# Optimization experiments

Measured on AMD Instinct MI355X. Metric: run time of the kernel, lower is better.

Reference implementation:

```python
import jax, jax.numpy as jnp
import numpy as np

B, S, DIN, DOUT = 4, 2048, 2048, 8192


def setup_inputs() -> dict:
    key = jax.random.key(0)
    kx, kw = jax.random.split(key)
    x = jax.random.normal(kx, (B, S, DIN), dtype=jnp.float32)
    # match torch init: uniform(-bound, bound), bound = sqrt(3) * 0.5 * in_features**-0.5
    bound = (3.0 ** 0.5) * 0.5 * DIN ** (-0.5)
    weight = jax.random.uniform(kw, (DOUT, DIN), dtype=jnp.float32, minval=-bound, maxval=bound)
    return {"x": x, "weight": weight}


def _rms_norm(x):
    # F.rms_norm with no weight: eps defaults to finfo(dtype).eps
    eps = jnp.finfo(x.dtype).eps
    return x * jax.lax.rsqrt(jnp.mean(x * x, axis=-1, keepdims=True) + eps)


def _act_quant(xn):
    # per-token int8 symmetric quant/dequant
    scale = 127.0 / jnp.maximum(jnp.max(jnp.abs(xn), axis=-1, keepdims=True), 1e-5)
    return jnp.clip(jnp.round(xn * scale), -128.0, 127.0) / scale


def _weight_quant(w):
    # ternary weight quant/dequant with global abs-mean scale
    scale = 1.0 / jnp.maximum(jnp.mean(jnp.abs(w)), 1e-5)
    return jnp.clip(jnp.round(w * scale), -1.0, 1.0) / scale


def reference(x, weight):
    xn = _rms_norm(x)
    # STE: forward uses quantized values, gradient flows through xn / weight
    x_q = xn + jax.lax.stop_gradient(_act_quant(xn) - xn)
    w_q = weight + jax.lax.stop_gradient(_weight_quant(weight) - weight)
    # F.linear: x @ w.T  -> [B, S, DOUT]
    return jnp.einsum('bsd,od->bso', x_q, w_q)
```

## Files before the change

kernel.cpp:

```cpp
#include <hip/hip_runtime.h>

typedef unsigned int u32;
typedef int i32x4 __attribute__((ext_vector_type(4)));

#define DIN 2048
#define DOUT 8192
#define MROWS 8192
#define NELEM_W (8192 * 2048)
#define NT 16

#define WS_PART 0
#define WS_WFAC 16384
#define WS_ROWFAC 16640
#define WS_XQ 49408
#define WS_WQ (49408 + 16777216)

__global__ void k_wabs(const float* __restrict__ w, double* __restrict__ part) {
    const float4* w4 = (const float4*)w;
    const unsigned t = threadIdx.x, b = blockIdx.x;
    float s = 0.f;
    for (unsigned i = b * 256u + t; i < (NELEM_W / 4); i += 2048u * 256u) {
        float4 v = w4[i];
        s += fabsf(v.x) + fabsf(v.y) + fabsf(v.z) + fabsf(v.w);
    }
    double d = (double)s;
    #pragma unroll
    for (int o = 32; o; o >>= 1) d += __shfl_down(d, o);
    __shared__ double red[4];
    if ((t & 63u) == 0u) red[t >> 6] = d;
    __syncthreads();
    if (t == 0) part[b] = red[0] + red[1] + red[2] + red[3];
}

__global__ void k_wfin(const double* __restrict__ part, float* __restrict__ wfac) {
    const int t = threadIdx.x;
    double s = 0.0;
    #pragma unroll
    for (int j = 0; j < 8; ++j) s += part[t + j * 256];
    #pragma unroll
    for (int o = 32; o; o >>= 1) s += __shfl_down(s, o);
    __shared__ double red[4];
    if ((t & 63) == 0) red[t >> 6] = s;
    __syncthreads();
    if (t == 0) {
        double mean = (red[0] + red[1] + red[2] + red[3]) * (1.0 / (double)NELEM_W);
        *wfac = fmaxf((float)mean, 1e-5f);
    }
}

__global__ void k_prep(const float* __restrict__ w, const float* __restrict__ wfac,
                       u32* __restrict__ wq, const float* __restrict__ x,
                       u32* __restrict__ xq, float* __restrict__ rowfac) {
    const int t = threadIdx.x;
    if (blockIdx.x < 2048) {
        const float scale = 1.0f / *wfac;
        const float4* w4 = (const float4*)w;
        for (unsigned i = blockIdx.x * 256u + t; i < (NELEM_W / 4); i += 2048u * 256u) {
            float4 v = w4[i];
            int q0 = (int)fminf(fmaxf(rintf(v.x * scale), -1.f), 1.f);
            int q1 = (int)fminf(fmaxf(rintf(v.y * scale), -1.f), 1.f);
            int q2 = (int)fminf(fmaxf(rintf(v.z * scale), -1.f), 1.f);
            int q3 = (int)fminf(fmaxf(rintf(v.w * scale), -1.f), 1.f);
            wq[i] = (u32)(q0 & 255) | ((u32)(q1 & 255) << 8) |
                    ((u32)(q2 & 255) << 16) | ((u32)(q3 & 255) << 24);
        }
        return;
    }
    const int row = blockIdx.x - 2048;
    const float4* xr = (const float4*)(x + (size_t)row * DIN);
    float4 v0 = xr[t], v1 = xr[t + 256];
    float ss = v0.x * v0.x + v0.y * v0.y + v0.z * v0.z + v0.w * v0.w
             + v1.x * v1.x + v1.y * v1.y + v1.z * v1.z + v1.w * v1.w;
    __shared__ float red[4];
    #pragma unroll
    for (int o = 32; o; o >>= 1) ss += __shfl_down(ss, o);
    if ((t & 63) == 0) red[t >> 6] = ss;
    __syncthreads();
    ss = red[0] + red[1] + red[2] + red[3];
    const float r = 1.0f / sqrtf(ss * (1.0f / DIN) + 1.1920929e-7f);
    float xn[8] = {v0.x * r, v0.y * r, v0.z * r, v0.w * r,
                   v1.x * r, v1.y * r, v1.z * r, v1.w * r};
    float am = 0.f;
    #pragma unroll
    for (int j = 0; j < 8; ++j) am = fmaxf(am, fabsf(xn[j]));
    __syncthreads();
    #pragma unroll
    for (int o = 32; o; o >>= 1) am = fmaxf(am, __shfl_down(am, o));
    if ((t & 63) == 0) red[t >> 6] = am;
    __syncthreads();
    am = fmaxf(fmaxf(red[0], red[1]), fmaxf(red[2], red[3]));
    const float amc = fmaxf(am, 1e-5f);
    const float s = 127.0f / amc;
    int q[8];
    #pragma unroll
    for (int j = 0; j < 8; ++j)
        q[j] = (int)fminf(fmaxf(rintf(xn[j] * s), -128.f), 127.f);
    u32* xo = xq + (size_t)row * (DIN / 4);
    xo[t] = (u32)(q[0] & 255) | ((u32)(q[1] & 255) << 8) |
            ((u32)(q[2] & 255) << 16) | ((u32)(q[3] & 255) << 24);
    xo[t + 256] = (u32)(q[4] & 255) | ((u32)(q[5] & 255) << 8) |
                  ((u32)(q[6] & 255) << 16) | ((u32)(q[7] & 255) << 24);
    if (t == 0) rowfac[row] = amc * (1.0f / 127.0f);
}

__launch_bounds__(512, 2)
__global__ void k_gemm(const char* __restrict__ A, const char* __restrict__ Bw,
                       const float* __restrict__ rowfac, const float* __restrict__ wfac,
                       float* __restrict__ out) {
    __shared__ __attribute__((aligned(16))) char smb[131072];

    const int t = threadIdx.x;
    const int l = t & 63, w = t >> 6;
    const int wm = w >> 2, wn = w & 3;
    const int lr = l & 15, lc = l >> 4;
    const int laneF = lr * 64 + ((lc ^ ((lr >> 1) & 3)) * 16);

    const int bid = blockIdx.x;
    const int xcd = bid & 7, idx = bid >> 3;
    const int st = xcd * 32 + idx;
    const int sm = st >> 4, sn = st & 15;

    const float wf = *wfac;

#define STAGE(gbase, opOff, tB, kh, s) do {                                       \
    _Pragma("unroll")                                                             \
    for (int j_ = 0; j_ < 2; ++j_) {                                              \
        const int seg_ = w * 2 + j_;                                              \
        const int row_ = seg_ * 16 + (l >> 2);                                    \
        const int sc_ = (l & 3) ^ ((l >> 3) & 3);                                 \
        const char* src_ = (gbase) + (size_t)row_ * DIN + (tB) + (kh) * 64 + sc_ * 16; \
        __builtin_amdgcn_global_load_lds(                                         \
            (const __attribute__((address_space(1))) void*)src_,                  \
            (__attribute__((address_space(3))) void*)(smb + (opOff) + (s) * 32768 + (kh) * 16384 + seg_ * 1024), \
            16, 0, 0);                                                            \
    }                                                                             \
} while (0)

#define STGT(tB, s) do {                                                          \
    STAGE(Ab, 0,     (tB), 0, (s));                                               \
    STAGE(Bb, 65536, (tB), 0, (s));                                               \
    STAGE(Ab, 0,     (tB), 1, (s));                                               \
    STAGE(Bb, 65536, (tB), 1, (s));                                               \
} while (0)

#define RDA(s, kh, mB, dst) do {                                                  \
    _Pragma("unroll")                                                             \
    for (int i_ = 0; i_ < 4; ++i_)                                                \
        dst[i_] = *(const i32x4*)(smb + (s) * 32768 + (kh) * 16384 +              \
                                  (wm * 128 + ((mB) + i_) * 16) * 64 + laneF);    \
} while (0)

#define RDB(s, kh, dst) do {                                                      \
    _Pragma("unroll")                                                             \
    for (int n_ = 0; n_ < 4; ++n_)                                                \
        dst[n_] = *(const i32x4*)(smb + 65536 + (s) * 32768 + (kh) * 16384 +      \
                                  (wn * 64 + n_ * 16) * 64 + laneF);              \
} while (0)

#define MFMA16(mB, fA, fB) do {                                                   \
    __builtin_amdgcn_s_setprio(1);                                                \
    _Pragma("unroll")                                                             \
    for (int i_ = 0; i_ < 4; ++i_)                                                \
        _Pragma("unroll")                                                         \
        for (int n_ = 0; n_ < 4; ++n_)                                            \
            acc[(mB) + i_][n_] = __builtin_amdgcn_mfma_i32_16x16x64_i8(           \
                fA[i_], fB[n_], acc[(mB) + i_][n_], 0, 0, 0);                     \
    __builtin_amdgcn_s_setprio(0);                                                \
} while (0)

#define LGKM0 asm volatile("s_waitcnt lgkmcnt(0)" ::: "memory")
#define VM(n) asm volatile("s_waitcnt vmcnt(" #n ")" ::: "memory")
#define BAR __builtin_amdgcn_s_barrier()

#define TILE(s, o, STG_STMT, GATE_STMT) do {                                      \
    RDA(s, 0, 4, fa2);                                                            \
    RDB(s, 1, fb2);                                                               \
    MFMA16(0, fa, fb);                                              \
    RDA(s, 1, 0, fa);                                                             \
    MFMA16(4, fa2, fb);                                             \
    RDA(s, 1, 4, fa2);                                                            \
    MFMA16(0, fa, fb2);                                             \
    LGKM0;                                        \
    BAR;                                                                          \
    STG_STMT;                                       \
    GATE_STMT;                                        \
    BAR;                                                                          \
    RDB(o, 0, fb);                                           \
    RDA(o, 0, 0, fa);                                                             \
    MFMA16(4, fa2, fb2);                  \
} while (0)

    #pragma unroll 1
    for (int j = 0; j < 4; ++j) {
        const int bm = sm * 2 + (j >> 1);
        const int bn = sn * 2 + ((j & 1) ^ (j >> 1));
        const char* Ab = A + (size_t)(bm * 256) * DIN;
        const char* Bb = Bw + (size_t)(bn * 256) * DIN;

        i32x4 acc[8][4] = {};
        i32x4 fa[4], fa2[4], fb[4], fb2[4];

        BAR;
        STGT(0, 0);
        STGT(128, 1);
        VM(8);
        BAR;
        RDB(0, 0, fb);
        RDA(0, 0, 0, fa);

        #pragma unroll 1
        for (int it = 0; it < 7; ++it) {
            const int tB = it * 256;
            TILE(0, 1, STGT(tB + 256, 0), VM(8));
            TILE(1, 0, STGT(tB + 384, 1), VM(8));
        }
        TILE(0, 1, (void)0, VM(0));
        RDA(1, 0, 4, fa2);
        RDB(1, 1, fb2);
        MFMA16(0, fa, fb);
        RDA(1, 1, 0, fa);
        MFMA16(4, fa2, fb);
        RDA(1, 1, 4, fa2);
        MFMA16(0, fa, fb2);
        MFMA16(4, fa2, fb2);

        const int c0 = bn * 256 + wn * 64 + lr;
        #pragma unroll
        for (int m = 0; m < 8; ++m) {
            #pragma unroll
            for (int r = 0; r < 4; ++r) {
                const int grow = bm * 256 + wm * 128 + m * 16 + lc * 4 + r;
                const float s = rowfac[grow] * wf;
                const size_t ob = (size_t)grow * DOUT + c0;
                #pragma unroll
                for (int n = 0; n < 4; ++n)
                    out[ob + n * 16] = (float)acc[m][n][r] * s;
            }
        }
    }
#undef STAGE
#undef STGT
#undef RDA
#undef RDB
#undef MFMA16
#undef LGKM0
#undef VM
#undef BAR
#undef TILE
}

extern "C" void kernel_launch(void* const* d_in, const int* in_sizes, int n_in,
                              void* d_out, int out_size, void* d_ws, size_t ws_size,
                              hipStream_t stream) {
    const float* x = (const float*)d_in[0];
    const float* wt = (const float*)d_in[1];
    float* out = (float*)d_out;
    char* ws = (char*)d_ws;

    double* part = (double*)(ws + WS_PART);
    float* wfac = (float*)(ws + WS_WFAC);
    float* rowfac = (float*)(ws + WS_ROWFAC);
    u32* xq = (u32*)(ws + WS_XQ);
    u32* wq = (u32*)(ws + WS_WQ);

    k_wabs<<<2048, 256, 0, stream>>>(wt, part);
    k_wfin<<<1, 256, 0, stream>>>(part, wfac);
    k_prep<<<2048 + MROWS, 256, 0, stream>>>(wt, wfac, wq, x, xq, rowfac);
    k_gemm<<<256, 512, 0, stream>>>((const char*)xq, (const char*)wq, rowfac, wfac, out);
}
```

Measured before the change: 226.8 us.

## Shrink GEMM tile to 256x128 with one tile per block and higher occupancy

```diff
diff --git a/kernel.cpp b/kernel.cpp
--- a/kernel.cpp
+++ b/kernel.cpp
@@ -7,7 +7,6 @@
 #define DOUT 8192
 #define MROWS 8192
 #define NELEM_W (8192 * 2048)
-#define NT 16
 
 #define WS_PART 0
 #define WS_WFAC 16384
@@ -103,68 +102,51 @@
     if (t == 0) rowfac[row] = amc * (1.0f / 127.0f);
 }
 
-__launch_bounds__(512, 2)
+__launch_bounds__(512, 4)
 __global__ void k_gemm(const char* __restrict__ A, const char* __restrict__ Bw,
                        const float* __restrict__ rowfac, const float* __restrict__ wfac,
                        float* __restrict__ out) {
-    __shared__ __attribute__((aligned(16))) char smb[131072];
+    __shared__ __attribute__((aligned(16))) char smb[49152];
 
     const int t = threadIdx.x;
     const int l = t & 63, w = t >> 6;
-    const int wm = w >> 2, wn = w & 3;
+    const int wm = w >> 1, wn = w & 1;
     const int lr = l & 15, lc = l >> 4;
     const int laneF = lr * 64 + ((lc ^ ((lr >> 1) & 3)) * 16);
+    const int srow = t >> 2;
+    const int sgl = ((t & 3) ^ ((t >> 3) & 3)) * 16;
 
     const int bid = blockIdx.x;
-    const int xcd = bid & 7, idx = bid >> 3;
-    const int st = xcd * 32 + idx;
-    const int sm = st >> 4, sn = st & 15;
-
-    const float wf = *wfac;
-
-#define STAGE(gbase, opOff, tB, kh, s) do {                                       \
+    const int g = (bid & 7) * 256 + (bid >> 3);
+    const int bm = g >> 6, bn = g & 63;
+    const char* Ab = A + (size_t)(bm * 256) * DIN;
+    const char* Bb = Bw + (size_t)(bn * 128) * DIN;
+
+    i32x4 acc[4][4] = {};
+    i32x4 fb[4], fa01[2], fa23[2];
+
+#define STG(tB, s) do {                                                           \
     _Pragma("unroll")                                                             \
-    for (int j_ = 0; j_ < 2; ++j_) {                                              \
-        const int seg_ = w * 2 + j_;                                              \
-        const int row_ = seg_ * 16 + (l >> 2);                                    \
-        const int sc_ = (l & 3) ^ ((l >> 3) & 3);                                 \
-        const char* src_ = (gbase) + (size_t)row_ * DIN + (tB) + (kh) * 64 + sc_ * 16; \
+    for (int j_ = 0; j_ < 2; ++j_)                                                \
         __builtin_amdgcn_global_load_lds(                                         \
-            (const __attribute__((address_space(1))) void*)src_,                  \
-            (__attribute__((address_space(3))) void*)(smb + (opOff) + (s) * 32768 + (kh) * 16384 + seg_ * 1024), \
-            16, 0, 0);                                                            \
-    }                                                                             \
+            (const __attribute__((address_space(1))) void*)(Ab + (size_t)(j_ * 128 + srow) * DIN + (tB) + sgl), \
+            (__attribute__((address_space(3))) void*)(smb + (s) * 16384 + j_ * 8192 + t * 16), 16, 0, 0); \
+    __builtin_amdgcn_global_load_lds(                                             \
+        (const __attribute__((address_space(1))) void*)(Bb + (size_t)srow * DIN + (tB) + sgl), \
+        (__attribute__((address_space(3))) void*)(smb + 32768 + (s) * 8192 + t * 16), 16, 0, 0); \
 } while (0)
 
-#define STGT(tB, s) do {                                                          \
-    STAGE(Ab, 0,     (tB), 0, (s));                                               \
-    STAGE(Bb, 65536, (tB), 0, (s));                                               \
-    STAGE(Ab, 0,     (tB), 1, (s));                                               \
-    STAGE(Bb, 65536, (tB), 1, (s));                                               \
-} while (0)
-
-#define RDA(s, kh, mB, dst) do {                                                  \
-    _Pragma("unroll")                                                             \
-    for (int i_ = 0; i_ < 4; ++i_)                                                \
-        dst[i_] = *(const i32x4*)(smb + (s) * 32768 + (kh) * 16384 +              \
-                                  (wm * 128 + ((mB) + i_) * 16) * 64 + laneF);    \
-} while (0)
-
-#define RDB(s, kh, dst) do {                                                      \
-    _Pragma("unroll")                                                             \
-    for (int n_ = 0; n_ < 4; ++n_)                                                \
-        dst[n_] = *(const i32x4*)(smb + 65536 + (s) * 32768 + (kh) * 16384 +      \
-                                  (wn * 64 + n_ * 16) * 64 + laneF);              \
-} while (0)
-
-#define MFMA16(mB, fA, fB) do {                                                   \
+#define RDA(s, m_) (*(const i32x4*)(smb + (s) * 16384 + (wm * 64 + (m_) * 16) * 64 + laneF))
+#define RDB(s, n_) (*(const i32x4*)(smb + 32768 + (s) * 8192 + (wn * 64 + (n_) * 16) * 64 + laneF))
+
+#define MFMA_G(mB, fA) do {                                                       \
     __builtin_amdgcn_s_setprio(1);                                                \
     _Pragma("unroll")                                                             \
-    for (int i_ = 0; i_ < 4; ++i_)                                                \
+    for (int i_ = 0; i_ < 2; ++i_)                                                \
         _Pragma("unroll")                                                         \
         for (int n_ = 0; n_ < 4; ++n_)                                            \
             acc[(mB) + i_][n_] = __builtin_amdgcn_mfma_i32_16x16x64_i8(           \
-                fA[i_], fB[n_], acc[(mB) + i_][n_], 0, 0, 0);                     \
+                fA[i_], fb[n_], acc[(mB) + i_][n_], 0, 0, 0);                     \
     __builtin_amdgcn_s_setprio(0);                                                \
 } while (0)
 
@@ -173,76 +155,58 @@
 #define BAR __builtin_amdgcn_s_barrier()
 
 #define TILE(s, o, STG_STMT, GATE_STMT) do {                                      \
-    RDA(s, 0, 4, fa2);                                                            \
-    RDB(s, 1, fb2);                                                               \
-    MFMA16(0, fa, fb);                                              \
-    RDA(s, 1, 0, fa);                                                             \
-    MFMA16(4, fa2, fb);                                             \
-    RDA(s, 1, 4, fa2);                                                            \
-    MFMA16(0, fa, fb2);                                             \
-    LGKM0;                                        \
-    BAR;                                                                          \
-    STG_STMT;                                       \
+    LGKM0;                                         \
+    BAR;                                            \
+    STG_STMT;                                                       \
     GATE_STMT;                                        \
     BAR;                                                                          \
-    RDB(o, 0, fb);                                           \
-    RDA(o, 0, 0, fa);                                                             \
-    MFMA16(4, fa2, fb2);                  \
+    MFMA_G(0, fa01);                                    \
+    fa01[0] = RDA(o, 0);                                                          \
+    fa01[1] = RDA(o, 1);                   \
+    MFMA_G(2, fa23);                              \
+    fa23[0] = RDA(o, 2);                                                          \
+    fa23[1] = RDA(o, 3);                                                          \
+    fb[0] = RDB(o, 0); fb[1] = RDB(o, 1);                                         \
+    fb[2] = RDB(o, 2); fb[3] = RDB(o, 3);           \
 } while (0)
 
+    STG(0, 0);
+    STG(64, 1);
+    VM(3);
+    BAR;
+    fb[0] = RDB(0, 0); fb[1] = RDB(0, 1); fb[2] = RDB(0, 2); fb[3] = RDB(0, 3);
+    fa01[0] = RDA(0, 0); fa01[1] = RDA(0, 1);
+    fa23[0] = RDA(0, 2); fa23[1] = RDA(0, 3);
+
     #pragma unroll 1
-    for (int j = 0; j < 4; ++j) {
-        const int bm = sm * 2 + (j >> 1);
-        const int bn = sn * 2 + ((j & 1) ^ (j >> 1));
-        const char* Ab = A + (size_t)(bm * 256) * DIN;
-        const char* Bb = Bw + (size_t)(bn * 256) * DIN;
-
-        i32x4 acc[8][4] = {};
-        i32x4 fa[4], fa2[4], fb[4], fb2[4];
-
-        BAR;
-        STGT(0, 0);
-        STGT(128, 1);
-        VM(8);
-        BAR;
-        RDB(0, 0, fb);
-        RDA(0, 0, 0, fa);
-
-        #pragma unroll 1
-        for (int it = 0; it < 7; ++it) {
-            const int tB = it * 256;
-            TILE(0, 1, STGT(tB + 256, 0), VM(8));
-            TILE(1, 0, STGT(tB + 384, 1), VM(8));
+    for (int p = 0; p < 15; ++p) {
+        const int tB = p * 128;
+        TILE(0, 1, STG(tB + 128, 0), VM(3));
+        TILE(1, 0, STG(tB + 192, 1), VM(3));
+    }
+    TILE(0, 1, (void)0, VM(0));
+    LGKM0;
+    MFMA_G(0, fa01);
+    MFMA_G(2, fa23);
+
+    const float wf = *wfac;
+    const int c0 = bn * 128 + wn * 64 + lr;
+    #pragma unroll
+    for (int m = 0; m < 4; ++m) {
+        #pragma unroll
+        for (int r = 0; r < 4; ++r) {
+            const int grow = bm * 256 + wm * 64 + m * 16 + lc * 4 + r;
+            const float s = rowfac[grow] * wf;
+            const size_t ob = (size_t)grow * DOUT + c0;
+            #pragma unroll
+            for (int n = 0; n < 4; ++n)
+                out[ob + n * 16] = (float)acc[m][n][r] * s;
         }
-        TILE(0, 1, (void)0, VM(0));
-        RDA(1, 0, 4, fa2);
-        RDB(1, 1, fb2);
-        MFMA16(0, fa, fb);
-        RDA(1, 1, 0, fa);
-        MFMA16(4, fa2, fb);
-        RDA(1, 1, 4, fa2);
-        MFMA16(0, fa, fb2);
-        MFMA16(4, fa2, fb2);
-
-        const int c0 = bn * 256 + wn * 64 + lr;
-        #pragma unroll
-        for (int m = 0; m < 8; ++m) {
-            #pragma unroll
-            for (int r = 0; r < 4; ++r) {
-                const int grow = bm * 256 + wm * 128 + m * 16 + lc * 4 + r;
-                const float s = rowfac[grow] * wf;
-                const size_t ob = (size_t)grow * DOUT + c0;
-                #pragma unroll
-                for (int n = 0; n < 4; ++n)
-                    out[ob + n * 16] = (float)acc[m][n][r] * s;
-            }
-        }
-    }
-#undef STAGE
-#undef STGT
+    }
+#undef STG
 #undef RDA
 #undef RDB
-#undef MFMA16
+#undef MFMA_G
 #undef LGKM0
 #undef VM
 #undef BAR
@@ -266,5 +230,5 @@
     k_wabs<<<2048, 256, 0, stream>>>(wt, part);
     k_wfin<<<1, 256, 0, stream>>>(part, wfac);
     k_prep<<<2048 + MROWS, 256, 0, stream>>>(wt, wfac, wq, x, xq, rowfac);
-    k_gemm<<<256, 512, 0, stream>>>((const char*)xq, (const char*)wq, rowfac, wfac, out);
-}
+    k_gemm<<<2048, 512, 0, stream>>>((const char*)xq, (const char*)wq, rowfac, wfac, out);
+}
```

Result: faster. 213.8 us (-5.7%).
